# Kernel tuning notes

Measured on AMD Instinct MI355X. Metric: run time of the kernel, lower is better.

Reference implementation:

```python
import jax, jax.numpy as jnp
import numpy as np

EPS_CLAMP = 1.0 - 1e-06


def _patch_pool_view(x, H, W, p):
    # x: (n, H*W, s) with spatial flattened row-major over (H, W)
    # -> (n, (H//p)*(W//p), p*p, s), matching einops 'n (h ph w pw) s -> n (h w) (ph pw) s'
    n, q, s = x.shape
    h, w = H // p, W // p
    x = x.reshape(n, h, p, w, p, s)
    x = x.transpose(0, 1, 3, 2, 4, 5)  # n h w ph pw s
    return x.reshape(n, h * w, p * p, s)


def setup_inputs() -> dict:
    key = jax.random.key(0)
    k1, k2 = jax.random.split(key)
    N, C, H, W = 8, 256, 48, 48
    return {
        'mask_feats': jax.random.normal(k1, (N, C, H, W), dtype=jnp.float32),
        'query_feats_all': jax.random.normal(k2, (N, C, H, W), dtype=jnp.float32),
        'path_size': 4,
    }


def reference(mask_feats, query_feats_all, path_size):
    N, c_m, hm, wm = mask_feats.shape
    _, c_q, hq, wq = query_feats_all.shape
    # n c h w -> n (h w) c, scaled by 1/sqrt(c)
    mf = mask_feats.reshape(N, c_m, hm * wm).transpose(0, 2, 1) / (c_m ** 0.5)
    qf = query_feats_all.reshape(N, c_q, hq * wq).transpose(0, 2, 1) / (c_q ** 0.5)
    sim_matrix = jnp.einsum('nqc,nsc->nqs', qf, mf) * 10.0  # (N, Q, S)
    instance_masks = jax.nn.softmax(sim_matrix, axis=1)
    query_masks = jnp.swapaxes(jax.nn.softmax(sim_matrix, axis=2), 1, 2)  # (N, S, Q)
    # patch pooling (computed under torch.no_grad in original)
    tmp_instance_masks_d = jax.lax.stop_gradient(
        _patch_pool_view(instance_masks, hq, wq, path_size))
    instance_masks_d = jnp.minimum(tmp_instance_masks_d.sum(axis=2), EPS_CLAMP)
    tmp_query_masks_d = jax.lax.stop_gradient(
        _patch_pool_view(query_masks, hm, wm, path_size))
    query_masks_d = jnp.minimum(tmp_query_masks_d.sum(axis=2), EPS_CLAMP)
    return (instance_masks, query_masks, instance_masks_d, query_masks_d,
            tmp_instance_masks_d, tmp_query_masks_d)
```

## Files before the change

kernel.cpp:

```cpp
#include <hip/hip_runtime.h>
#include <hip/hip_bf16.h>

#define N_B 8
#define CH 256
#define HW 2304
#define SZ_QS (2304LL*2304LL)
#define SCALE 0.0390625f
#define EPSC 0.999999f
#define QS 512.0f
#define IQS 0.001953125f

typedef __attribute__((ext_vector_type(8))) short bf8_t;
typedef __attribute__((ext_vector_type(8))) unsigned short u16x8;
typedef __attribute__((ext_vector_type(4))) float f32x4;

#define O1 0LL
#define O2 42467328LL
#define O3 84934656LL
#define O4 87588864LL
#define O5 90243072LL
#define O6 132710400LL

__device__ __forceinline__ void gl_lds16(const unsigned short* g, unsigned short* l) {
  __builtin_amdgcn_global_load_lds(
      (const __attribute__((address_space(1))) unsigned int*)g,
      (__attribute__((address_space(3))) unsigned int*)l, 16, 0, 0);
}

__global__ __launch_bounds__(256) void k_tr(const float* __restrict__ q_in,
                                            const float* __restrict__ m_in,
                                            __hip_bfloat16* __restrict__ Abf,
                                            __hip_bfloat16* __restrict__ Bbf,
                                            float* __restrict__ zbuf) {
  __shared__ float lds[64][65];
  const int n = blockIdx.z >> 1, which = blockIdx.z & 1;
  const float* src = which ? m_in : q_in;
  __hip_bfloat16* dst = which ? Bbf : Abf;
  const int q0 = blockIdx.x * 64, c0 = blockIdx.y * 64;
  const int t = threadIdx.x;

  if (zbuf && blockIdx.y == 0 && blockIdx.z == 0) {
    const int i = (blockIdx.x * 256 + t) * 4;
    *(float4*)(zbuf + i) = make_float4(0.f, 0.f, 0.f, 0.f);
  }

  const int cl4 = t >> 4, q4 = (t & 15) * 4;
#pragma unroll
  for (int p = 0; p < 4; ++p) {
    const int cl = p * 16 + cl4;
    const float4 v = *(const float4*)(src + ((size_t)n * CH + c0 + cl) * HW + q0 + q4);
    lds[cl][q4 + 0] = v.x;
    lds[cl][q4 + 1] = v.y;
    lds[cl][q4 + 2] = v.z;
    lds[cl][q4 + 3] = v.w;
  }
  __syncthreads();

  const int c8 = (t & 7) * 8;
#pragma unroll
  for (int p = 0; p < 2; ++p) {
    const int ql = p * 32 + (t >> 3);
    u16x8 o;
#pragma unroll
    for (int k = 0; k < 8; ++k) {
      const __hip_bfloat16 h = __float2bfloat16(lds[c8 + k][ql]);
      o[k] = *(const unsigned short*)&h;
    }
    *(u16x8*)((unsigned short*)dst + ((size_t)n * HW + q0 + ql) * CH + c0 + c8) = o;
  }
}

__global__ __launch_bounds__(256) void k_zero(float* __restrict__ p) {
  const int i = (blockIdx.x * 256 + threadIdx.x) * 4;
  *(float4*)(p + i) = make_float4(0.f, 0.f, 0.f, 0.f);
}

__global__ __launch_bounds__(256) void k_inv(const float* __restrict__ s,
                                             float* __restrict__ inv,
                                             const float scale) {
  const int i = blockIdx.x * 256 + threadIdx.x;
  inv[i] = scale / s[i];
}

__global__ __launch_bounds__(512) void k_p1(
    const unsigned short* __restrict__ Abf, const unsigned short* __restrict__ Bbf,
    float* __restrict__ out1, float* __restrict__ rowsum, float* __restrict__ colsum) {
  __shared__ unsigned short smem[4 * 192 * 32];

  const int n = blockIdx.z;
  const int S0 = blockIdx.x * 192, Q0 = blockIdx.y * 192;
  const int t = threadIdx.x, l = t & 63, w = t >> 6;
  const int wm = w >> 2, wn = w & 3;
  const int g = l >> 4, c = l & 15;

  f32x4 acc[6][3];
#pragma unroll
  for (int mi = 0; mi < 6; ++mi)
#pragma unroll
    for (int ni = 0; ni < 3; ++ni) {
      f32x4 z = {0.f, 0.f, 0.f, 0.f};
      acc[mi][ni] = z;
    }

  const int rrel = l >> 2;
  const int sseg = (l & 3) ^ ((l >> 3) & 3);
  const unsigned short* gAb = Abf + ((size_t)n * HW + Q0) * CH;
  const unsigned short* gBb = Bbf + ((size_t)n * HW + S0) * CH;
  const int ch0 = w * 3, ch1 = w * 3 + 1, ch2 = w * 3 + 2;

#define STAGE_CHUNK(chv, buf, k0)                                              \
  {                                                                            \
    const int isA = (chv) < 12;                                                \
    const int crel = isA ? (chv) : (chv)-12;                                   \
    const unsigned short* sp_ =                                                \
        (isA ? gAb : gBb) + (size_t)(crel * 16 + rrel) * CH + (k0) + sseg * 8; \
    unsigned short* dp_ = smem + (buf)*12288 + (isA ? 0 : 6144) + crel * 512;  \
    gl_lds16(sp_, dp_);                                                        \
  }

#define STAGE_STEP(buf, step)                  \
  {                                            \
    const int k0_ = (step)*32;                 \
    STAGE_CHUNK(ch0, buf, k0_);                \
    STAGE_CHUNK(ch1, buf, k0_);                \
    STAGE_CHUNK(ch2, buf, k0_);                \
  }

  STAGE_STEP(0, 0);
  __syncthreads();

  int cur = 0;
#pragma unroll 2
  for (int step = 0; step < 8; ++step) {
    if (step < 7) STAGE_STEP(cur ^ 1, step + 1);
    const unsigned short* lA = smem + cur * 12288;
    const unsigned short* lB = lA + 6144;
    bf8_t af[6], bf_[3];
#pragma unroll
    for (int mi = 0; mi < 6; ++mi) {
      const int r = wm * 96 + mi * 16 + c;
      const int sg_ = g ^ ((c >> 1) & 3);
      af[mi] = *(const bf8_t*)(lA + r * 32 + sg_ * 8);
    }
#pragma unroll
    for (int ni = 0; ni < 3; ++ni) {
      const int r = wn * 48 + ni * 16 + c;
      const int sg_ = g ^ ((c >> 1) & 3);
      bf_[ni] = *(const bf8_t*)(lB + r * 32 + sg_ * 8);
    }
#pragma unroll
    for (int mi = 0; mi < 6; ++mi)
#pragma unroll
      for (int ni = 0; ni < 3; ++ni)
        acc[mi][ni] = __builtin_amdgcn_mfma_f32_16x16x32_bf16(af[mi], bf_[ni], acc[mi][ni], 0, 0, 0);
    __syncthreads();
    cur ^= 1;
  }
#undef STAGE_CHUNK
#undef STAGE_STEP

#pragma unroll
  for (int mi = 0; mi < 6; ++mi)
#pragma unroll
    for (int ni = 0; ni < 3; ++ni)
#pragma unroll
      for (int r = 0; r < 4; ++r)
        acc[mi][ni][r] = __expf(acc[mi][ni][r] * SCALE);

  u16x8 ud[9];
#pragma unroll
  for (int mi = 0; mi < 6; ++mi)
#pragma unroll
    for (int ni = 0; ni < 3; ++ni)
#pragma unroll
      for (int r = 0; r < 4; ++r) {
        const int L = mi * 12 + ni * 4 + r;
        ud[L >> 3][L & 7] =
            (unsigned short)fminf(acc[mi][ni][r] * QS + 0.5f, 65535.0f);
      }
  {
    const size_t base = ((size_t)n * HW + Q0) * HW + S0;
#pragma unroll
    for (int j = 0; j < 9; ++j) {
      const int chunk = j * 512 + t;
      const int row = chunk / 48, c16 = chunk % 48;
      *(u16x8*)(out1 + base + (size_t)row * HW + c16 * 4) = ud[j];
    }
  }

#pragma unroll
  for (int mi = 0; mi < 6; ++mi)
#pragma unroll
    for (int r = 0; r < 4; ++r) {
      float v = acc[mi][0][r] + acc[mi][1][r] + acc[mi][2][r];
      v += __shfl_xor(v, 1, 64);
      v += __shfl_xor(v, 2, 64);
      v += __shfl_xor(v, 4, 64);
      v += __shfl_xor(v, 8, 64);
      if (c == 0) atomicAdd(&rowsum[n * HW + Q0 + wm * 96 + mi * 16 + g * 4 + r], v);
    }
#pragma unroll
  for (int ni = 0; ni < 3; ++ni) {
    float v = 0.f;
#pragma unroll
    for (int mi = 0; mi < 6; ++mi)
#pragma unroll
      for (int r = 0; r < 4; ++r) v += acc[mi][ni][r];
    v += __shfl_xor(v, 16, 64);
    v += __shfl_xor(v, 32, 64);
    if (g == 0) atomicAdd(&colsum[n * HW + S0 + wn * 48 + ni * 16 + c], v);
  }
}

__global__ __launch_bounds__(512) void k_p2(
    float* __restrict__ out1, float* __restrict__ out2, float* __restrict__ out3,
    float* __restrict__ out4, float* __restrict__ out5, float* __restrict__ out6,
    const float* __restrict__ rowsum, const float* __restrict__ colsum) {
  __shared__ float fb[48 * 196];
  const int n = blockIdx.z;
  const int bx = blockIdx.x, hq = blockIdx.y;
  const int S0 = bx * 192, Q0 = hq * 192;
  const int t = threadIdx.x, l = t & 63, w = t >> 6;
  const int wm = w >> 2, wn = w & 3;
  const int g = l >> 4, c = l & 15;

  u16x8 ud[9];
  {
    const size_t base = ((size_t)n * HW + Q0) * HW + S0;
#pragma unroll
    for (int j = 0; j < 9; ++j) {
      const int chunk = j * 512 + t;
      const int row = chunk / 48, c16 = chunk % 48;
      ud[j] = *(const u16x8*)(out1 + base + (size_t)row * HW + c16 * 4);
    }
  }
  f32x4 acc[6][3];
#pragma unroll
  for (int mi = 0; mi < 6; ++mi)
#pragma unroll
    for (int ni = 0; ni < 3; ++ni)
#pragma unroll
      for (int r = 0; r < 4; ++r) {
        const int L = mi * 12 + ni * 4 + r;
        acc[mi][ni][r] = (float)ud[L >> 3][L & 7];
      }

  float icv[3];
#pragma unroll
  for (int ni = 0; ni < 3; ++ni)
    icv[ni] = IQS / colsum[n * HW + S0 + wn * 48 + ni * 16 + c];
  f32x4 irv6[6];
#pragma unroll
  for (int mi = 0; mi < 6; ++mi) {
    const int qloc = wm * 96 + mi * 16 + g * 4;
    const f32x4 rs = *(const f32x4*)(rowsum + n * HW + Q0 + qloc);
#pragma unroll
    for (int r = 0; r < 4; ++r) irv6[mi][r] = IQS / rs[r];
  }

#pragma unroll
  for (int ch = 0; ch < 4; ++ch) {
    if (wm == (ch >> 1)) {
#pragma unroll
      for (int m3 = 0; m3 < 3; ++m3) {
        const int mi = (ch & 1) * 3 + m3;
        const int rowb = m3 * 16 + g * 4;
#pragma unroll
        for (int ni = 0; ni < 3; ++ni) {
          const int colb = wn * 48 + ni * 16 + c;
#pragma unroll
          for (int r = 0; r < 4; ++r)
            fb[(rowb + r) * 196 + colb] = acc[mi][ni][r] * icv[ni];
        }
      }
    }
    __syncthreads();
#pragma unroll
    for (int j = 0; j < 5; ++j) {
      const int idx = t + j * 512;
      if (idx < 2304) {
        const int row = idx / 48, col4 = idx % 48;
        const float4 v = *(const float4*)(fb + row * 196 + col4 * 4);
        *(float4*)(out1 + ((size_t)n * HW + Q0 + ch * 48 + row) * HW + S0 + col4 * 4) = v;
        const size_t r5 = ((size_t)n * 144 + hq * 12 + (row >> 2)) * 16 + ch * 4 + (row & 3);
        *(float4*)(out5 + r5 * HW + S0 + col4 * 4) = v;
      }
    }
    __syncthreads();
  }

#pragma unroll
  for (int ch = 0; ch < 4; ++ch) {
    if (wn == ch) {
#pragma unroll
      for (int mi = 0; mi < 6; ++mi) {
        const int colf = wm * 96 + mi * 16 + g * 4;
#pragma unroll
        for (int ni = 0; ni < 3; ++ni) {
          const f32x4 pq = acc[mi][ni] * irv6[mi];
          *(f32x4*)(fb + (ni * 16 + c) * 196 + colf) = pq;
        }
      }
    }
    __syncthreads();
#pragma unroll
    for (int j = 0; j < 5; ++j) {
      const int idx = t + j * 512;
      if (idx < 2304) {
        const int row = idx / 48, col4 = idx % 48;
        const float4 v = *(const float4*)(fb + row * 196 + col4 * 4);
        *(float4*)(out2 + ((size_t)n * HW + S0 + ch * 48 + row) * HW + Q0 + col4 * 4) = v;
        const size_t r6 = ((size_t)n * 144 + bx * 12 + (row >> 2)) * 16 + ch * 4 + (row & 3);
        *(float4*)(out6 + r6 * HW + Q0 + col4 * 4) = v;
      }
    }
    __syncthreads();
  }

#pragma unroll
  for (int m3 = 0; m3 < 3; ++m3) {
    const int b = m3 * 4 + g;
#pragma unroll
    for (int ni = 0; ni < 3; ++ni) {
      const int sl = wn * 48 + ni * 16 + c;
      float p = 0.f;
#pragma unroll
      for (int r = 0; r < 4; ++r) p += acc[m3][ni][r] + acc[m3 + 3][ni][r];
      fb[(wm * 12 + b) * 196 + sl] = p * icv[ni];
    }
  }
  __syncthreads();
#pragma unroll
  for (int j = 0; j < 5; ++j) {
    const int idx = t + j * 512;
    if (idx < 2304) {
      const int b = idx / 192, sl = idx % 192;
      const float v = fb[b * 196 + sl] + fb[(12 + b) * 196 + sl];
      out3[((size_t)n * 144 + hq * 12 + b) * HW + S0 + sl] = fminf(v, EPSC);
    }
  }
  __syncthreads();

#pragma unroll
  for (int mi = 0; mi < 6; ++mi) {
    const int qloc = wm * 96 + mi * 16 + g * 4;
#pragma unroll
    for (int ni = 0; ni < 3; ++ni) {
      f32x4 pq = acc[mi][ni] * irv6[mi];
#pragma unroll
      for (int r = 0; r < 4; ++r) {
        pq[r] += __shfl_xor(pq[r], 1, 64);
        pq[r] += __shfl_xor(pq[r], 2, 64);
      }
      if ((c & 3) == 0) {
        const int pc = ni * 4 + (c >> 2);
        *(f32x4*)(fb + (wn * 12 + pc) * 196 + qloc) = pq;
      }
    }
  }
  __syncthreads();
#pragma unroll
  for (int j = 0; j < 5; ++j) {
    const int idx = t + j * 512;
    if (idx < 2304) {
      const int pc = idx / 192, q = idx % 192;
      const float v = fb[pc * 196 + q] + fb[(12 + pc) * 196 + q] +
                      fb[(24 + pc) * 196 + q] + fb[(36 + pc) * 196 + q];
      out4[((size_t)n * 144 + bx * 12 + pc) * HW + Q0 + q] = fminf(v, EPSC);
    }
  }
}

__global__ __launch_bounds__(256) void k_gemm_old(const unsigned short* __restrict__ Abf,
                                                  const unsigned short* __restrict__ Bbf,
                                                  float* __restrict__ out1,
                                                  float* __restrict__ rowsum,
                                                  float* __restrict__ colsum) {
  __shared__ unsigned short lA[128 * 64];
  __shared__ unsigned short lB[128 * 64];
  const int n = blockIdx.z;
  const int s0 = blockIdx.x * 128, q0 = blockIdx.y * 128;
  const int t = threadIdx.x, l = t & 63, w = t >> 6;
  const int wm = w >> 1, wn = w & 1;
  f32x4 acc[4][4];
#pragma unroll
  for (int mi = 0; mi < 4; ++mi)
#pragma unroll
    for (int ni = 0; ni < 4; ++ni) {
      f32x4 z = {0.f, 0.f, 0.f, 0.f};
      acc[mi][ni] = z;
    }
  const size_t baseA = ((size_t)n * HW + q0) * CH;
  const size_t baseB = ((size_t)n * HW + s0) * CH;
  const int jj = t & 7, rr = t >> 3;
  for (int kc = 0; kc < 4; ++kc) {
    const int k0 = kc * 64;
#pragma unroll
    for (int i = 0; i < 4; ++i) {
      const int r = i * 32 + rr;
      bf8_t va = *(const bf8_t*)(Abf + baseA + (size_t)r * CH + k0 + jj * 8);
      bf8_t vb = *(const bf8_t*)(Bbf + baseB + (size_t)r * CH + k0 + jj * 8);
      *(bf8_t*)(lA + r * 64 + ((jj ^ (r & 7)) * 8)) = va;
      *(bf8_t*)(lB + r * 64 + ((jj ^ (r & 7)) * 8)) = vb;
    }
    __syncthreads();
#pragma unroll
    for (int ks = 0; ks < 2; ++ks) {
      const int kb = ks * 4 + (l >> 4);
      bf8_t af[4], bfr[4];
#pragma unroll
      for (int mi = 0; mi < 4; ++mi) {
        const int r = wm * 64 + mi * 16 + (l & 15);
        af[mi] = *(const bf8_t*)(lA + r * 64 + ((kb ^ (r & 7)) * 8));
      }
#pragma unroll
      for (int ni = 0; ni < 4; ++ni) {
        const int r = wn * 64 + ni * 16 + (l & 15);
        bfr[ni] = *(const bf8_t*)(lB + r * 64 + ((kb ^ (r & 7)) * 8));
      }
#pragma unroll
      for (int mi = 0; mi < 4; ++mi)
#pragma unroll
        for (int ni = 0; ni < 4; ++ni)
          acc[mi][ni] = __builtin_amdgcn_mfma_f32_16x16x32_bf16(af[mi], bfr[ni], acc[mi][ni], 0, 0, 0);
    }
    __syncthreads();
  }
  float rp[4][4], cp[4];
#pragma unroll
  for (int mi = 0; mi < 4; ++mi)
#pragma unroll
    for (int r = 0; r < 4; ++r) rp[mi][r] = 0.f;
#pragma unroll
  for (int ni = 0; ni < 4; ++ni) cp[ni] = 0.f;
#pragma unroll
  for (int mi = 0; mi < 4; ++mi) {
    const int row = q0 + wm * 64 + mi * 16 + (l >> 4) * 4;
#pragma unroll
    for (int ni = 0; ni < 4; ++ni) {
      const int col = s0 + wn * 64 + ni * 16 + (l & 15);
      const size_t ob = ((size_t)n * HW + row) * HW + col;
#pragma unroll
      for (int r = 0; r < 4; ++r) {
        const float e = __expf(acc[mi][ni][r] * SCALE);
        out1[ob + (size_t)r * HW] = e;
        rp[mi][r] += e;
        cp[ni] += e;
      }
    }
  }
#pragma unroll
  for (int mi = 0; mi < 4; ++mi)
#pragma unroll
    for (int r = 0; r < 4; ++r) {
      float v = rp[mi][r];
      v += __shfl_xor(v, 1, 64);
      v += __shfl_xor(v, 2, 64);
      v += __shfl_xor(v, 4, 64);
      v += __shfl_xor(v, 8, 64);
      if ((l & 15) == 0)
        atomicAdd(&rowsum[n * HW + q0 + wm * 64 + mi * 16 + (l >> 4) * 4 + r], v);
    }
#pragma unroll
  for (int ni = 0; ni < 4; ++ni) {
    float v = cp[ni];
    v += __shfl_xor(v, 16, 64);
    v += __shfl_xor(v, 32, 64);
    if (l < 16) atomicAdd(&colsum[n * HW + s0 + wn * 64 + ni * 16 + l], v);
  }
}

__global__ __launch_bounds__(192) void k_main(float* __restrict__ out1,
                                              float* __restrict__ out2,
                                              float* __restrict__ out3,
                                              float* __restrict__ out5,
                                              float* __restrict__ out6,
                                              const float* __restrict__ invr,
                                              const float* __restrict__ invc) {
  __shared__ float ldsT[192 * 49];
  const int n = blockIdx.z, h = blockIdx.y, sb = blockIdx.x;
  const int S0 = sb * 192;
  const int t = threadIdx.x;
  const int sg = S0 + t;
  const float icv = invc[n * HW + sg];
  const float* invr_n = invr + n * HW;
  float* e_base = out1 + (size_t)n * SZ_QS;
  const int Q0 = h * 192;
  float acc[12];
#pragma unroll
  for (int i = 0; i < 12; ++i) acc[i] = 0.f;
  for (int ph = 0; ph < 4; ++ph) {
    const int qf0 = Q0 + ph * 48;
#pragma unroll
    for (int wi = 0; wi < 12; ++wi) {
#pragma unroll
      for (int pw = 0; pw < 4; ++pw) {
        const int col = wi * 4 + pw;
        const int q = qf0 + col;
        const size_t eoff = (size_t)q * HW + sg;
        const float e = e_base[eoff];
        const float pi = e * icv;
        e_base[eoff] = pi;
        out5[((size_t)((n * 144 + h * 12 + wi) * 16 + (ph * 4 + pw))) * HW + sg] = pi;
        acc[wi] += pi;
        ldsT[t * 49 + col] = e * invr_n[q];
      }
    }
    __syncthreads();
    const int u = t & 3, sB = t >> 2;
#pragma unroll
    for (int pass = 0; pass < 4; ++pass) {
      const int sl = pass * 48 + sB;
      const int sgl = S0 + sl;
      const int rs_ = sgl / 48, cs = sgl % 48;
      const int sp = (rs_ >> 2) * 12 + (cs >> 2);
      const int spp = (rs_ & 3) * 4 + (cs & 3);
      const size_t o2row = ((size_t)n * HW + sgl) * HW + qf0;
      const size_t o6row = (((size_t)n * 144 + sp) * 16 + spp) * HW + qf0;
#pragma unroll
      for (int k = 0; k < 3; ++k) {
        const int slot = u + k * 4;
        float4 v;
        v.x = ldsT[sl * 49 + slot * 4 + 0];
        v.y = ldsT[sl * 49 + slot * 4 + 1];
        v.z = ldsT[sl * 49 + slot * 4 + 2];
        v.w = ldsT[sl * 49 + slot * 4 + 3];
        *(float4*)(out2 + o2row + slot * 4) = v;
        *(float4*)(out6 + o6row + slot * 4) = v;
      }
    }
    __syncthreads();
  }
#pragma unroll
  for (int wi = 0; wi < 12; ++wi)
    out3[((size_t)(n * 144 + h * 12 + wi)) * HW + sg] = fminf(acc[wi], EPSC);
}

__global__ __launch_bounds__(256) void k_qd(const float* __restrict__ out6,
                                            float* __restrict__ out4) {
  const int n = blockIdx.y, sp = blockIdx.x;
  const float* b6 = out6 + (((size_t)n * 144 + sp) * 16) * HW;
  float* b4 = out4 + ((size_t)n * 144 + sp) * HW;
  for (int i = 0; i < 9; ++i) {
    const int qq = i * 256 + threadIdx.x;
    float s = 0.f;
#pragma unroll
    for (int spp = 0; spp < 16; ++spp) s += b6[(size_t)spp * HW + qq];
    b4[qq] = fminf(s, EPSC);
  }
}

extern "C" void kernel_launch(void* const* d_in, const int* in_sizes, int n_in,
                              void* d_out, int out_size, void* d_ws, size_t ws_size,
                              hipStream_t stream) {
  const float* mask_f = (const float*)d_in[0];
  const float* query_f = (const float*)d_in[1];
  float* out = (float*)d_out;
  float* out1 = out + O1;
  float* out2 = out + O2;
  float* out3 = out + O3;
  float* out4 = out + O4;
  float* out5 = out + O5;
  float* out6 = out + O6;

  const size_t abytes = (size_t)N_B * HW * CH * 2;
  const size_t sbytes = (size_t)N_B * HW * 4;
  const size_t need = 2 * abytes + 4 * sbytes;

  if (ws_size >= need) {
    char* base = (char*)d_ws;
    __hip_bfloat16* Abf = (__hip_bfloat16*)base;
    __hip_bfloat16* Bbf = (__hip_bfloat16*)(base + abytes);
    float* sums = (float*)(base + 2 * abytes);
    float* rowsum = sums;
    float* colsum = sums + N_B * HW;

    k_tr<<<dim3(36, 4, 16), 256, 0, stream>>>(query_f, mask_f, Abf, Bbf, sums);
    k_p1<<<dim3(12, 12, 8), 512, 0, stream>>>(
        (const unsigned short*)Abf, (const unsigned short*)Bbf, out1, rowsum, colsum);
    k_p2<<<dim3(12, 12, 8), 512, 0, stream>>>(out1, out2, out3, out4, out5, out6,
                                              rowsum, colsum);
  } else {
    __hip_bfloat16* Abf = (__hip_bfloat16*)out4;
    __hip_bfloat16* Bbf = (__hip_bfloat16*)out3;
    float* sums = (float*)((char*)out4 + abytes);
    float* invs = sums + 2 * (N_B * HW);
    float* rowsum = sums;
    float* colsum = sums + N_B * HW;
    float* invr = invs;
    float* invc = invs + N_B * HW;

    k_tr<<<dim3(36, 4, 16), 256, 0, stream>>>(query_f, mask_f, Abf, Bbf, nullptr);
    k_zero<<<dim3(36), 256, 0, stream>>>(sums);
    k_gemm_old<<<dim3(18, 18, 8), 256, 0, stream>>>(
        (const unsigned short*)Abf, (const unsigned short*)Bbf, out1, rowsum, colsum);
    k_inv<<<dim3(144), 256, 0, stream>>>(sums, invs, 1.0f);
    k_main<<<dim3(12, 12, 8), 192, 0, stream>>>(out1, out2, out3, out5, out6, invr, invc);
    k_qd<<<dim3(144, 8), 256, 0, stream>>>(out6, out4);
  }
}
```

Before: 224.1 us.

## Recompute GEMM in second pass instead of storing quantized exp values

Previously pass 1 wrote exp(sim) as 16-bit quantized values into out1 and pass 2 read them back. Now pass 1 only computes the row and column sums, and pass 2 recomputes the bf16 GEMM and exp itself. This removes a large global write and read of the Q×S tile and the quantization error, at the cost of doing the MFMA GEMM twice. LDS is shared between the GEMM staging buffers and the pass-2 transpose buffer.

```diff
diff --git a/kernel.cpp b/kernel.cpp
--- a/kernel.cpp
+++ b/kernel.cpp
@@ -7,8 +7,6 @@
 #define SZ_QS (2304LL*2304LL)
 #define SCALE 0.0390625f
 #define EPSC 0.999999f
-#define QS 512.0f
-#define IQS 0.001953125f
 
 typedef __attribute__((ext_vector_type(8))) short bf8_t;
 typedef __attribute__((ext_vector_type(8))) unsigned short u16x8;
@@ -25,6 +23,85 @@
   __builtin_amdgcn_global_load_lds(
       (const __attribute__((address_space(1))) unsigned int*)g,
       (__attribute__((address_space(3))) unsigned int*)l, 16, 0, 0);
+}
+
+__device__ __forceinline__ void gemm192(
+    const unsigned short* __restrict__ Abf, const unsigned short* __restrict__ Bbf,
+    unsigned short* __restrict__ smem, const int n, const int S0, const int Q0,
+    const int t, f32x4 (&acc)[6][3]) {
+  const int l = t & 63, w = t >> 6;
+  const int wm = w >> 1 >> 1, wn = w & 3;
+  const int g = l >> 4, c = l & 15;
+
+#pragma unroll
+  for (int mi = 0; mi < 6; ++mi)
+#pragma unroll
+    for (int ni = 0; ni < 3; ++ni) {
+      f32x4 z = {0.f, 0.f, 0.f, 0.f};
+      acc[mi][ni] = z;
+    }
+
+  const int rrel = l >> 2;
+  const int sseg = (l & 3) ^ ((l >> 3) & 3);
+  const unsigned short* gAb = Abf + ((size_t)n * HW + Q0) * CH;
+  const unsigned short* gBb = Bbf + ((size_t)n * HW + S0) * CH;
+  const int ch0 = w * 3;
+
+#define STAGE_CHUNK(chv, buf, k0)                                              \
+  {                                                                            \
+    const int isA = (chv) < 12;                                                \
+    const int crel = isA ? (chv) : (chv)-12;                                   \
+    const unsigned short* sp_ =                                                \
+        (isA ? gAb : gBb) + (size_t)(crel * 16 + rrel) * CH + (k0) + sseg * 8; \
+    unsigned short* dp_ = smem + (buf)*12288 + (isA ? 0 : 6144) + crel * 512;  \
+    gl_lds16(sp_, dp_);                                                        \
+  }
+
+  STAGE_CHUNK(ch0 + 0, 0, 0);
+  STAGE_CHUNK(ch0 + 1, 0, 0);
+  STAGE_CHUNK(ch0 + 2, 0, 0);
+  __syncthreads();
+
+  int cur = 0;
+#pragma unroll 2
+  for (int step = 0; step < 8; ++step) {
+    if (step < 7) {
+      const int k0_ = (step + 1) * 32;
+      STAGE_CHUNK(ch0 + 0, cur ^ 1, k0_);
+      STAGE_CHUNK(ch0 + 1, cur ^ 1, k0_);
+      STAGE_CHUNK(ch0 + 2, cur ^ 1, k0_);
+    }
+    const unsigned short* lA = smem + cur * 12288;
+    const unsigned short* lB = lA + 6144;
+    bf8_t af[6], bf_[3];
+    const int sg_ = g ^ ((c >> 1) & 3);
+#pragma unroll
+    for (int mi = 0; mi < 6; ++mi) {
+      const int r = wm * 96 + mi * 16 + c;
+      af[mi] = *(const bf8_t*)(lA + r * 32 + sg_ * 8);
+    }
+#pragma unroll
+    for (int ni = 0; ni < 3; ++ni) {
+      const int r = wn * 48 + ni * 16 + c;
+      bf_[ni] = *(const bf8_t*)(lB + r * 32 + sg_ * 8);
+    }
+#pragma unroll
+    for (int mi = 0; mi < 6; ++mi)
+#pragma unroll
+      for (int ni = 0; ni < 3; ++ni)
+        acc[mi][ni] = __builtin_amdgcn_mfma_f32_16x16x32_bf16(af[mi], bf_[ni], acc[mi][ni], 0, 0, 0);
+    __syncthreads();
+    cur ^= 1;
+  }
+#undef STAGE_CHUNK
+
+#pragma unroll
+  for (int mi = 0; mi < 6; ++mi)
+#pragma unroll
+    for (int ni = 0; ni < 3; ++ni)
+#pragma unroll
+      for (int r = 0; r < 4; ++r)
+        acc[mi][ni][r] = __expf(acc[mi][ni][r] * SCALE);
 }
 
 __global__ __launch_bounds__(256) void k_tr(const float* __restrict__ q_in,
@@ -84,9 +161,8 @@
 
 __global__ __launch_bounds__(512) void k_p1(
     const unsigned short* __restrict__ Abf, const unsigned short* __restrict__ Bbf,
-    float* __restrict__ out1, float* __restrict__ rowsum, float* __restrict__ colsum) {
-  __shared__ unsigned short smem[4 * 192 * 32];
-
+    float* __restrict__ rowsum, float* __restrict__ colsum) {
+  __shared__ char smem[49152];
   const int n = blockIdx.z;
   const int S0 = blockIdx.x * 192, Q0 = blockIdx.y * 192;
   const int t = threadIdx.x, l = t & 63, w = t >> 6;
@@ -94,99 +170,7 @@
   const int g = l >> 4, c = l & 15;
 
   f32x4 acc[6][3];
-#pragma unroll
-  for (int mi = 0; mi < 6; ++mi)
-#pragma unroll
-    for (int ni = 0; ni < 3; ++ni) {
-      f32x4 z = {0.f, 0.f, 0.f, 0.f};
-      acc[mi][ni] = z;
-    }
-
-  const int rrel = l >> 2;
-  const int sseg = (l & 3) ^ ((l >> 3) & 3);
-  const unsigned short* gAb = Abf + ((size_t)n * HW + Q0) * CH;
-  const unsigned short* gBb = Bbf + ((size_t)n * HW + S0) * CH;
-  const int ch0 = w * 3, ch1 = w * 3 + 1, ch2 = w * 3 + 2;
-
-#define STAGE_CHUNK(chv, buf, k0)                                              \
-  {                                                                            \
-    const int isA = (chv) < 12;                                                \
-    const int crel = isA ? (chv) : (chv)-12;                                   \
-    const unsigned short* sp_ =                                                \
-        (isA ? gAb : gBb) + (size_t)(crel * 16 + rrel) * CH + (k0) + sseg * 8; \
-    unsigned short* dp_ = smem + (buf)*12288 + (isA ? 0 : 6144) + crel * 512;  \
-    gl_lds16(sp_, dp_);                                                        \
-  }
-
-#define STAGE_STEP(buf, step)                  \
-  {                                            \
-    const int k0_ = (step)*32;                 \
-    STAGE_CHUNK(ch0, buf, k0_);                \
-    STAGE_CHUNK(ch1, buf, k0_);                \
-    STAGE_CHUNK(ch2, buf, k0_);                \
-  }
-
-  STAGE_STEP(0, 0);
-  __syncthreads();
-
-  int cur = 0;
-#pragma unroll 2
-  for (int step = 0; step < 8; ++step) {
-    if (step < 7) STAGE_STEP(cur ^ 1, step + 1);
-    const unsigned short* lA = smem + cur * 12288;
-    const unsigned short* lB = lA + 6144;
-    bf8_t af[6], bf_[3];
-#pragma unroll
-    for (int mi = 0; mi < 6; ++mi) {
-      const int r = wm * 96 + mi * 16 + c;
-      const int sg_ = g ^ ((c >> 1) & 3);
-      af[mi] = *(const bf8_t*)(lA + r * 32 + sg_ * 8);
-    }
-#pragma unroll
-    for (int ni = 0; ni < 3; ++ni) {
-      const int r = wn * 48 + ni * 16 + c;
-      const int sg_ = g ^ ((c >> 1) & 3);
-      bf_[ni] = *(const bf8_t*)(lB + r * 32 + sg_ * 8);
-    }
-#pragma unroll
-    for (int mi = 0; mi < 6; ++mi)
-#pragma unroll
-      for (int ni = 0; ni < 3; ++ni)
-        acc[mi][ni] = __builtin_amdgcn_mfma_f32_16x16x32_bf16(af[mi], bf_[ni], acc[mi][ni], 0, 0, 0);
-    __syncthreads();
-    cur ^= 1;
-  }
-#undef STAGE_CHUNK
-#undef STAGE_STEP
-
-#pragma unroll
-  for (int mi = 0; mi < 6; ++mi)
-#pragma unroll
-    for (int ni = 0; ni < 3; ++ni)
-#pragma unroll
-      for (int r = 0; r < 4; ++r)
-        acc[mi][ni][r] = __expf(acc[mi][ni][r] * SCALE);
-
-  u16x8 ud[9];
-#pragma unroll
-  for (int mi = 0; mi < 6; ++mi)
-#pragma unroll
-    for (int ni = 0; ni < 3; ++ni)
-#pragma unroll
-      for (int r = 0; r < 4; ++r) {
-        const int L = mi * 12 + ni * 4 + r;
-        ud[L >> 3][L & 7] =
-            (unsigned short)fminf(acc[mi][ni][r] * QS + 0.5f, 65535.0f);
-      }
-  {
-    const size_t base = ((size_t)n * HW + Q0) * HW + S0;
-#pragma unroll
-    for (int j = 0; j < 9; ++j) {
-      const int chunk = j * 512 + t;
-      const int row = chunk / 48, c16 = chunk % 48;
-      *(u16x8*)(out1 + base + (size_t)row * HW + c16 * 4) = ud[j];
-    }
-  }
+  gemm192(Abf, Bbf, (unsigned short*)smem, n, S0, Q0, t, acc);
 
 #pragma unroll
   for (int mi = 0; mi < 6; ++mi)
@@ -213,10 +197,11 @@
 }
 
 __global__ __launch_bounds__(512) void k_p2(
+    const unsigned short* __restrict__ Abf, const unsigned short* __restrict__ Bbf,
     float* __restrict__ out1, float* __restrict__ out2, float* __restrict__ out3,
     float* __restrict__ out4, float* __restrict__ out5, float* __restrict__ out6,
     const float* __restrict__ rowsum, const float* __restrict__ colsum) {
-  __shared__ float fb[48 * 196];
+  __shared__ char smem[49152];
   const int n = blockIdx.z;
   const int bx = blockIdx.x, hq = blockIdx.y;
   const int S0 = bx * 192, Q0 = hq * 192;
@@ -224,38 +209,21 @@
   const int wm = w >> 2, wn = w & 3;
   const int g = l >> 4, c = l & 15;
 
-  u16x8 ud[9];
-  {
-    const size_t base = ((size_t)n * HW + Q0) * HW + S0;
-#pragma unroll
-    for (int j = 0; j < 9; ++j) {
-      const int chunk = j * 512 + t;
-      const int row = chunk / 48, c16 = chunk % 48;
-      ud[j] = *(const u16x8*)(out1 + base + (size_t)row * HW + c16 * 4);
-    }
-  }
   f32x4 acc[6][3];
-#pragma unroll
-  for (int mi = 0; mi < 6; ++mi)
-#pragma unroll
-    for (int ni = 0; ni < 3; ++ni)
-#pragma unroll
-      for (int r = 0; r < 4; ++r) {
-        const int L = mi * 12 + ni * 4 + r;
-        acc[mi][ni][r] = (float)ud[L >> 3][L & 7];
-      }
+  gemm192(Abf, Bbf, (unsigned short*)smem, n, S0, Q0, t, acc);
+  float* fb = (float*)smem;
 
   float icv[3];
 #pragma unroll
   for (int ni = 0; ni < 3; ++ni)
-    icv[ni] = IQS / colsum[n * HW + S0 + wn * 48 + ni * 16 + c];
+    icv[ni] = 1.0f / colsum[n * HW + S0 + wn * 48 + ni * 16 + c];
   f32x4 irv6[6];
 #pragma unroll
   for (int mi = 0; mi < 6; ++mi) {
     const int qloc = wm * 96 + mi * 16 + g * 4;
     const f32x4 rs = *(const f32x4*)(rowsum + n * HW + Q0 + qloc);
 #pragma unroll
-    for (int r = 0; r < 4; ++r) irv6[mi][r] = IQS / rs[r];
+    for (int r = 0; r < 4; ++r) irv6[mi][r] = 1.0f / rs[r];
   }
 
 #pragma unroll
@@ -577,9 +545,10 @@
 
     k_tr<<<dim3(36, 4, 16), 256, 0, stream>>>(query_f, mask_f, Abf, Bbf, sums);
     k_p1<<<dim3(12, 12, 8), 512, 0, stream>>>(
-        (const unsigned short*)Abf, (const unsigned short*)Bbf, out1, rowsum, colsum);
-    k_p2<<<dim3(12, 12, 8), 512, 0, stream>>>(out1, out2, out3, out4, out5, out6,
-                                              rowsum, colsum);
+        (const unsigned short*)Abf, (const unsigned short*)Bbf, rowsum, colsum);
+    k_p2<<<dim3(12, 12, 8), 512, 0, stream>>>(
+        (const unsigned short*)Abf, (const unsigned short*)Bbf,
+        out1, out2, out3, out4, out5, out6, rowsum, colsum);
   } else {
     __hip_bfloat16* Abf = (__hip_bfloat16*)out4;
     __hip_bfloat16* Bbf = (__hip_bfloat16*)out3;
```

New measurement: 224.9 us. No clear change (+0.3%).
